# Kernel tuning notes

Measured on AMD Instinct MI355X. Metric: run time of the kernel, lower is better.

Reference implementation:

```python
import jax, jax.numpy as jnp
import numpy as np

# Dims (match init_kwargs / module defaults)
RD, PD = 128, 64          # residue_dim, pair_dim
H, QD, VD = 12, 32, 32    # num_heads, q_dim, v_dim
QP, VP = 8, 8             # num_q_points, num_v_points
LN_EPS = 1e-5
DIR_EPS = 1e-4
INF = 1e5


def _layer_norm(x, g, b):
    m = x.mean(-1, keepdims=True)
    v = ((x - m) ** 2).mean(-1, keepdims=True)
    return (x - m) * jax.lax.rsqrt(v + LN_EPS) * g + b


def setup_inputs() -> dict:
    key = jax.random.key(0)
    ks = jax.random.split(key, 24)
    N, L = 2, 512
    inp = {}
    inp['R'] = jax.random.normal(ks[0], (N, L, 3, 3), jnp.float32)
    inp['coord'] = jax.random.normal(ks[1], (N, L, 3), jnp.float32)
    inp['residue_feat'] = jax.random.normal(ks[2], (N, L, RD), jnp.float32)
    inp['pair_feat'] = jax.random.normal(ks[3], (N, L, L, PD), jnp.float32)
    inp['mask'] = jax.random.randint(ks[4], (N, L), 0, 2).astype(bool)

    def lin(k, fan_in, fan_out):  # torch nn.Linear default init, weight (out, in)
        lim = 1.0 / np.sqrt(fan_in)
        return jax.random.uniform(k, (fan_out, fan_in), jnp.float32, -lim, lim)

    inp['Wq'] = lin(ks[5], RD, QD * H)
    inp['Wk'] = lin(ks[6], RD, QD * H)
    inp['Wv'] = lin(ks[7], RD, VD * H)
    inp['Wpb'] = lin(ks[8], PD, H)
    inp['spatial_coef'] = jnp.full((1, 1, 1, H), np.log(np.exp(1.0) - 1.0), jnp.float32)
    inp['Wqp'] = lin(ks[9], RD, QP * H * 3)
    inp['Wkp'] = lin(ks[10], RD, QP * H * 3)
    inp['Wvp'] = lin(ks[11], RD, VP * H * 3)
    in_feat = H * VD + H * PD + H * VP * (3 + 3 + 1)  # 1824
    inp['Wout'] = lin(ks[12], in_feat, RD)
    inp['bout'] = jnp.zeros((RD,), jnp.float32)
    inp['Wm1'] = lin(ks[13], RD, RD)
    inp['bm1'] = jnp.zeros((RD,), jnp.float32)
    inp['Wm2'] = lin(ks[14], RD, RD)
    inp['bm2'] = jnp.zeros((RD,), jnp.float32)
    inp['Wm3'] = lin(ks[15], RD, RD)
    inp['bm3'] = jnp.zeros((RD,), jnp.float32)
    inp['ln1_g'] = jnp.ones((RD,), jnp.float32)
    inp['ln1_b'] = jnp.zeros((RD,), jnp.float32)
    inp['ln2_g'] = jnp.ones((RD,), jnp.float32)
    inp['ln2_b'] = jnp.zeros((RD,), jnp.float32)
    return inp


def _forward(R, coord, residue_feat, pair_feat, mask,
             Wq, Wk, Wv, Wpb, spatial_coef, Wqp, Wkp, Wvp,
             Wout, bout, Wm1, bm1, Wm2, bm2, Wm3, bm3,
             ln1_g, ln1_b, ln2_g, ln2_b):
    N, L, _ = residue_feat.shape

    def l2g(p):  # local->global: R @ p + t ; p: (N,L,M,3)
        return jnp.einsum('nlij,nlmj->nlmi', R, p) + coord[:, :, None, :]

    # --- node logits ---
    q = (residue_feat @ Wq.T).reshape(N, L, H, QD)
    k = (residue_feat @ Wk.T).reshape(N, L, H, QD)
    logits_node = jnp.einsum('nihd,njhd->nijh', q, k) * (1.0 / np.sqrt(QD))

    # --- pair logits ---
    logits_pair = pair_feat @ Wpb.T  # (N,L,L,H)

    # --- spatial logits ---
    qp = l2g((residue_feat @ Wqp.T).reshape(N, L, H * QP, 3)).reshape(N, L, H, QP * 3)
    kp = l2g((residue_feat @ Wkp.T).reshape(N, L, H * QP, 3)).reshape(N, L, H, QP * 3)
    # ||q_i - k_j||^2 = |q|^2 + |k|^2 - 2 q.k (avoids (N,L,L,H,3P) intermediate)
    qq = (qp ** 2).sum(-1)  # (N,L,H)
    kk = (kp ** 2).sum(-1)
    sum_sq = qq[:, :, None] + kk[:, None] - 2.0 * jnp.einsum('nihd,njhd->nijh', qp, kp)
    gamma = jax.nn.softplus(spatial_coef)  # (1,1,1,H)
    logits_spatial = sum_sq * (-gamma * np.sqrt(2.0 / (9.0 * QP)) / 2.0)

    logits = (logits_node + logits_pair + logits_spatial) * np.sqrt(1.0 / 3.0)

    # --- masked softmax over key axis (dim=2) ---
    mask_row = mask[:, :, None, None]            # (N,L,1,1)
    mask_pair = mask_row & mask[:, None, :, None]
    logits = jnp.where(mask_pair, logits, logits - INF)
    alpha = jax.nn.softmax(logits, axis=2)
    alpha = jnp.where(mask_row, alpha, 0.0)      # (N,L,L,H)

    # --- node aggregation ---
    v = (residue_feat @ Wv.T).reshape(N, L, H, VD)
    feat_node = jnp.einsum('nijh,njhd->nihd', alpha, v).reshape(N, L, H * VD)

    # --- pair aggregation ---
    feat_pair = jnp.einsum('nijh,nijc->nihc', alpha, pair_feat).reshape(N, L, H * PD)

    # --- spatial aggregation ---
    vp = l2g((residue_feat @ Wvp.T).reshape(N, L, H * VP, 3)).reshape(N, L, H, VP, 3)
    aggr = jnp.einsum('nijh,njhpc->nihpc', alpha, vp)  # (N,L,H,VP,3) global frame
    diff = aggr - coord[:, :, None, None, :]
    feat_points = jnp.einsum('nlji,nlhpj->nlhpi', R, diff)  # global->local: R^T (x - t)
    feat_dist = jnp.sqrt((feat_points ** 2).sum(-1))        # (N,L,H,VP)
    feat_dir = feat_points / (feat_dist[..., None] + DIR_EPS)
    feat_spatial = jnp.concatenate([
        feat_points.reshape(N, L, -1),
        feat_dist.reshape(N, L, -1),
        feat_dir.reshape(N, L, -1),
    ], axis=-1)

    feat_all = jnp.concatenate([feat_pair, feat_node, feat_spatial], axis=-1)
    feat_all = feat_all @ Wout.T + bout
    feat_all = jnp.where(mask[:, :, None], feat_all, 0.0)

    x = _layer_norm(residue_feat + feat_all, ln1_g, ln1_b)
    mlp = jax.nn.relu(jax.nn.relu(x @ Wm1.T + bm1) @ Wm2.T + bm2) @ Wm3.T + bm3
    return _layer_norm(x + mlp, ln2_g, ln2_b)


def reference(R, coord, residue_feat, pair_feat, mask,
              Wq, Wk, Wv, Wpb, spatial_coef, Wqp, Wkp, Wvp,
              Wout, bout, Wm1, bm1, Wm2, bm2, Wm3, bm3,
              ln1_g, ln1_b, ln2_g, ln2_b):
    return _forward(R, coord, residue_feat, pair_feat, mask,
                    Wq, Wk, Wv, Wpb, spatial_coef, Wqp, Wkp, Wvp,
                    Wout, bout, Wm1, bm1, Wm2, bm2, Wm3, bm3,
                    ln1_g, ln1_b, ln2_g, ln2_b)
```

## Files before the change

kernel.cpp:

```cpp
#include <hip/hip_runtime.h>
#include <hip/hip_bf16.h>

#define N_ 2
#define L_ 512
#define RD_ 128
#define PD_ 64
#define H_ 12
#define NL_ (N_*L_)
#define POUT_ 2016
#define FEAT_ 1824
#define INF_ 100000.0f
#define ISQD_ 0.17677669529663687f
#define ISQ3_ 0.5773502691896258f
#define LL_ ((size_t)L_*L_)

__global__ __launch_bounds__(256) void k_proj_gemm(
    const float* __restrict__ resf,
    const float* __restrict__ Wq, const float* __restrict__ Wk, const float* __restrict__ Wv,
    const float* __restrict__ Wqp, const float* __restrict__ Wkp, const float* __restrict__ Wvp,
    float* __restrict__ proj)
{
  const int rb = blockIdx.x * 8;
  const int ob = blockIdx.y * 128;
  const int tid = threadIdx.x;
  __shared__ float xt[8*132];
  __shared__ float wt[128*132];
  {
    int r = tid >> 5, kq = (tid & 31) * 4;
    float4 v = *(const float4*)(resf + (size_t)(rb + r)*RD_ + kq);
    xt[r*132+kq]=v.x; xt[r*132+kq+1]=v.y; xt[r*132+kq+2]=v.z; xt[r*132+kq+3]=v.w;
  }
  for (int m = 0; m < 16; ++m) {
    int idx = m*256 + tid;
    int r = idx >> 5, kq = (idx & 31) * 4;
    int o = ob + r;
    float4 v;
    if (o < 384)        v = *(const float4*)(Wq  + (size_t)o*RD_ + kq);
    else if (o < 768)   v = *(const float4*)(Wk  + (size_t)(o-384)*RD_ + kq);
    else if (o < 1152)  v = *(const float4*)(Wv  + (size_t)(o-768)*RD_ + kq);
    else if (o < 1440)  v = *(const float4*)(Wqp + (size_t)(o-1152)*RD_ + kq);
    else if (o < 1728)  v = *(const float4*)(Wkp + (size_t)(o-1440)*RD_ + kq);
    else if (o < POUT_) v = *(const float4*)(Wvp + (size_t)(o-1728)*RD_ + kq);
    else                v = make_float4(0.f,0.f,0.f,0.f);
    wt[r*132+kq]=v.x; wt[r*132+kq+1]=v.y; wt[r*132+kq+2]=v.z; wt[r*132+kq+3]=v.w;
  }
  __syncthreads();
  const int tt = tid & 7, g = tid >> 3;
  float acc0=0.f, acc1=0.f, acc2=0.f, acc3=0.f;
  #pragma unroll 4
  for (int k2 = 0; k2 < RD_; ++k2) {
    float xv = xt[tt*132 + k2];
    acc0 += xv * wt[(g     )*132 + k2];
    acc1 += xv * wt[(g + 32)*132 + k2];
    acc2 += xv * wt[(g + 64)*132 + k2];
    acc3 += xv * wt[(g + 96)*132 + k2];
  }
  float* dst = proj + (size_t)(rb + tt)*POUT_ + ob;
  if (ob + g      < POUT_) dst[g]      = acc0;
  if (ob + g + 32 < POUT_) dst[g+32]   = acc1;
  if (ob + g + 64 < POUT_) dst[g+64]   = acc2;
  if (ob + g + 96 < POUT_) dst[g+96]   = acc3;
}

__global__ __launch_bounds__(64) void k_rot(
    const float* __restrict__ R, const float* __restrict__ coord,
    const float* __restrict__ spc, const float* __restrict__ proj,
    float* __restrict__ qt, float* __restrict__ kt, float* __restrict__ vpg)
{
  const int t = blockIdx.x;
  const int n = t / L_, i = t % L_;
  const int tid = threadIdx.x;
  __shared__ float prow[POUT_];
  __shared__ float qpl[288], kpl[288], vpl[288];
  __shared__ float qqs[H_], kks[H_], coefs[H_];
  for (int m = tid; m < POUT_/4; m += 64)
    ((float4*)prow)[m] = *((const float4*)(proj + (size_t)t*POUT_) + m);
  if (tid < H_) coefs[tid] = -log1pf(expf(spc[tid])) * (1.0f/12.0f);
  __syncthreads();
  const float* Rm = R + (size_t)t*9;
  const float r00=Rm[0],r01=Rm[1],r02=Rm[2],r10=Rm[3],r11=Rm[4],r12=Rm[5],r20=Rm[6],r21=Rm[7],r22=Rm[8];
  const float cx = coord[(size_t)t*3], cy = coord[(size_t)t*3+1], cz = coord[(size_t)t*3+2];
  for (int idx = tid; idx < 288; idx += 64) {
    int mat = idx / 96, p = idx % 96;
    const float* s = prow + 1152 + mat*288 + p*3;
    float px=s[0], py=s[1], pz=s[2];
    float gx = r00*px + r01*py + r02*pz + cx;
    float gy = r10*px + r11*py + r12*pz + cy;
    float gz = r20*px + r21*py + r22*pz + cz;
    float* d = (mat==0? qpl : mat==1? kpl : vpl) + p*3;
    d[0]=gx; d[1]=gy; d[2]=gz;
  }
  __syncthreads();
  if (tid < 24) {
    int mat = tid / H_, h = tid % H_;
    const float* s = (mat==0? qpl : kpl) + h*24;
    float acc = 0.f;
    #pragma unroll
    for (int c2 = 0; c2 < 24; ++c2) acc += s[c2]*s[c2];
    (mat==0? qqs : kks)[h] = acc;
  }
  for (int m = tid; m < 72; m += 64)
    ((float4*)(vpg + (size_t)t*288))[m] = ((float4*)vpl)[m];
  __syncthreads();
  for (int idx = tid; idx < 2*H_*64; idx += 64) {
    int which = idx / 768, rem = idx % 768, h = rem >> 6, c = rem & 63;
    float val;
    if (which == 0) {
      if (c < 32)       val = prow[h*32 + c] * ISQD_;
      else if (c < 56)  val = qpl[h*24 + (c-32)] * (-2.0f * coefs[h]);
      else if (c == 56) val = coefs[h] * qqs[h];
      else if (c == 57) val = coefs[h];
      else              val = 0.f;
      qt[((size_t)(n*H_ + h)*L_ + i)*64 + c] = val;
    } else {
      if (c < 32)       val = prow[384 + h*32 + c];
      else if (c < 56)  val = kpl[h*24 + (c-32)];
      else if (c == 56) val = 1.0f;
      else if (c == 57) val = kks[h];
      else              val = 0.f;
      kt[((size_t)(n*H_ + h)*L_ + i)*64 + c] = val;
    }
  }
}

__global__ __launch_bounds__(256) void k_lgns(
    const float* __restrict__ qt, const float* __restrict__ kt,
    float* __restrict__ lgal)
{
  const int jb = blockIdx.x * 64, ib = blockIdx.y * 64, nh = blockIdx.z;
  const int tid = threadIdx.x;
  __shared__ float qs[64*66], ks[64*66];
  for (int m = 0; m < 4; ++m) {
    int idx = m*256 + tid;
    int r = idx >> 4, kq = (idx & 15) * 4;
    float4 a = *(const float4*)(qt + ((size_t)nh*L_ + ib + r)*64 + kq);
    qs[r*66+kq]=a.x; qs[r*66+kq+1]=a.y; qs[r*66+kq+2]=a.z; qs[r*66+kq+3]=a.w;
    float4 b = *(const float4*)(kt + ((size_t)nh*L_ + jb + r)*64 + kq);
    ks[r*66+kq]=b.x; ks[r*66+kq+1]=b.y; ks[r*66+kq+2]=b.z; ks[r*66+kq+3]=b.w;
  }
  __syncthreads();
  const int tx = tid & 15, ty = tid >> 4;
  const int i0 = ty*4, j0 = tx*4;
  float acc[4][4] = {};
  #pragma unroll 4
  for (int k2 = 0; k2 < 64; k2 += 2) {
    float2 qv[4], kv[4];
    #pragma unroll
    for (int d = 0; d < 4; ++d) {
      qv[d] = *(const float2*)(qs + (i0+d)*66 + k2);
      kv[d] = *(const float2*)(ks + (j0+d)*66 + k2);
    }
    #pragma unroll
    for (int a2 = 0; a2 < 4; ++a2)
      #pragma unroll
      for (int b2 = 0; b2 < 4; ++b2)
        acc[a2][b2] += qv[a2].x*kv[b2].x + qv[a2].y*kv[b2].y;
  }
  #pragma unroll
  for (int a2 = 0; a2 < 4; ++a2) {
    float4 v = make_float4(acc[a2][0], acc[a2][1], acc[a2][2], acc[a2][3]);
    *(float4*)(lgal + ((size_t)nh*L_ + ib + i0 + a2)*L_ + jb + j0) = v;
  }
}

__global__ __launch_bounds__(256) void k_pbias(
    const float* __restrict__ pair, const int* __restrict__ mask,
    const float* __restrict__ Wpb, float* __restrict__ lgal)
{
  const int jt2 = blockIdx.x, i = blockIdx.y, n = blockIdx.z;
  const int bi = n*L_ + i;
  const int tid = threadIdx.x;
  __shared__ float pt[2][64*67];
  const int sr = tid >> 4, scq = (tid & 15)*4;
  #pragma unroll
  for (int m = 0; m < 4; ++m) {
    int r = m*16 + sr;
    float4 v = *(const float4*)(pair + ((size_t)bi*L_ + jt2*128 + r)*PD_ + scq);
    float* d = pt[0] + r*67 + scq;
    d[0]=v.x; d[1]=v.y; d[2]=v.z; d[3]=v.w;
  }
  __syncthreads();
  float4 rg[4];
  #pragma unroll
  for (int m = 0; m < 4; ++m) {
    int r = m*16 + sr;
    rg[m] = *(const float4*)(pair + ((size_t)bi*L_ + jt2*128 + 64 + r)*PD_ + scq);
  }

  const int r = tid & 63;
  const int w = __builtin_amdgcn_readfirstlane(tid >> 6);
  const float* w0 = Wpb + (w    )*64;
  const float* w1 = Wpb + (w + 4)*64;
  const float* w2 = Wpb + (w + 8)*64;
  const int mi = mask[bi];

  {
    const int j = jt2*128 + r;
    const float* pr = pt[0] + r*67;
    float a0=0.f, a1=0.f, a2=0.f;
    #pragma unroll 16
    for (int c = 0; c < 64; ++c) {
      float pv = pr[c];
      a0 += pv*w0[c]; a1 += pv*w1[c]; a2 += pv*w2[c];
    }
    const float mt = (mi && mask[n*L_ + j]) ? 0.f : -INF_;
    size_t base = ((size_t)(n*H_ + w)*L_ + i)*L_ + j;
    float l0 = lgal[base], l1 = lgal[base + 4*LL_], l2 = lgal[base + 8*LL_];
    lgal[base        ] = (l0 + a0)*ISQ3_ + mt;
    lgal[base + 4*LL_] = (l1 + a1)*ISQ3_ + mt;
    lgal[base + 8*LL_] = (l2 + a2)*ISQ3_ + mt;
  }

  #pragma unroll
  for (int m = 0; m < 4; ++m) {
    int rr = m*16 + sr;
    float* d = pt[1] + rr*67 + scq;
    d[0]=rg[m].x; d[1]=rg[m].y; d[2]=rg[m].z; d[3]=rg[m].w;
  }
  __syncthreads();
  {
    const int j = jt2*128 + 64 + r;
    const float* pr = pt[1] + r*67;
    float a0=0.f, a1=0.f, a2=0.f;
    #pragma unroll 16
    for (int c = 0; c < 64; ++c) {
      float pv = pr[c];
      a0 += pv*w0[c]; a1 += pv*w1[c]; a2 += pv*w2[c];
    }
    const float mt = (mi && mask[n*L_ + j]) ? 0.f : -INF_;
    size_t base = ((size_t)(n*H_ + w)*L_ + i)*L_ + j;
    float l0 = lgal[base], l1 = lgal[base + 4*LL_], l2 = lgal[base + 8*LL_];
    lgal[base        ] = (l0 + a0)*ISQ3_ + mt;
    lgal[base + 4*LL_] = (l1 + a1)*ISQ3_ + mt;
    lgal[base + 8*LL_] = (l2 + a2)*ISQ3_ + mt;
  }
}

__global__ __launch_bounds__(256) void k_softx(
    const int* __restrict__ mask, float* __restrict__ lgal)
{
  const int tid = threadIdx.x;
  const int wid = tid >> 6, lane = tid & 63;
  const int rid = blockIdx.x*4 + wid;
  const int i = rid & (L_-1);
  const int nh = rid >> 9;
  const int n = nh / H_;
  float4* r4 = (float4*)(lgal + (size_t)rid * L_);
  float4 p0 = r4[lane], p1 = r4[lane + 64];
  float mx = fmaxf(fmaxf(fmaxf(p0.x,p0.y),fmaxf(p0.z,p0.w)),
                   fmaxf(fmaxf(p1.x,p1.y),fmaxf(p1.z,p1.w)));
  #pragma unroll
  for (int off = 1; off < 64; off <<= 1) mx = fmaxf(mx, __shfl_xor(mx, off, 64));
  p0.x = expf(p0.x - mx); p0.y = expf(p0.y - mx);
  p0.z = expf(p0.z - mx); p0.w = expf(p0.w - mx);
  p1.x = expf(p1.x - mx); p1.y = expf(p1.y - mx);
  p1.z = expf(p1.z - mx); p1.w = expf(p1.w - mx);
  float s = p0.x+p0.y+p0.z+p0.w + p1.x+p1.y+p1.z+p1.w;
  #pragma unroll
  for (int off = 1; off < 64; off <<= 1) s += __shfl_xor(s, off, 64);
  const float inv = (mask[n*L_ + i] ? 1.f : 0.f) / s;
  p0.x*=inv; p0.y*=inv; p0.z*=inv; p0.w*=inv;
  p1.x*=inv; p1.y*=inv; p1.z*=inv; p1.w*=inv;
  r4[lane] = p0; r4[lane + 64] = p1;
}

__global__ __launch_bounds__(256) void k_paggr(
    const float* __restrict__ pair, const float* __restrict__ lgal,
    float* __restrict__ feat)
{
  const int i = blockIdx.x, n = blockIdx.y;
  const int bi = n*L_ + i;
  const int tid = threadIdx.x;
  const int w = tid >> 6, l = tid & 63;
  const int js = l >> 4, cq = (l & 15) << 2;
  __shared__ float part[4][H_][64];

  const float* pb = pair + ((size_t)bi*L_ + w*128 + js)*PD_ + cq;
  const float* ab[H_];
  #pragma unroll
  for (int h = 0; h < H_; ++h)
    ab[h] = lgal + ((size_t)(n*H_ + h)*L_ + i)*L_ + w*128 + js;

  float4 acc[H_];
  #pragma unroll
  for (int h = 0; h < H_; ++h) acc[h] = make_float4(0.f,0.f,0.f,0.f);

  #pragma unroll 2
  for (int g = 0; g < 32; ++g) {
    float4 pv = *(const float4*)(pb + (size_t)g*4*PD_);
    #pragma unroll
    for (int h = 0; h < H_; ++h) {
      float av = ab[h][g*4];
      acc[h].x += av*pv.x; acc[h].y += av*pv.y;
      acc[h].z += av*pv.z; acc[h].w += av*pv.w;
    }
  }

  #pragma unroll
  for (int h = 0; h < H_; ++h) {
    acc[h].x += __shfl_xor(acc[h].x, 16, 64);
    acc[h].y += __shfl_xor(acc[h].y, 16, 64);
    acc[h].z += __shfl_xor(acc[h].z, 16, 64);
    acc[h].w += __shfl_xor(acc[h].w, 16, 64);
    acc[h].x += __shfl_xor(acc[h].x, 32, 64);
    acc[h].y += __shfl_xor(acc[h].y, 32, 64);
    acc[h].z += __shfl_xor(acc[h].z, 32, 64);
    acc[h].w += __shfl_xor(acc[h].w, 32, 64);
  }
  if (l < 16) {
    #pragma unroll
    for (int h = 0; h < H_; ++h)
      *(float4*)(&part[w][h][cq]) = acc[h];
  }
  __syncthreads();
  for (int u = tid; u < H_*64; u += 256) {
    int h = u >> 6, c = u & 63;
    feat[(size_t)bi*FEAT_ + h*64 + c] =
        part[0][h][c] + part[1][h][c] + part[2][h][c] + part[3][h][c];
  }
}

__global__ __launch_bounds__(256) void k_av(
    const float* __restrict__ lgal, const float* __restrict__ proj,
    const float* __restrict__ vpg, float* __restrict__ pav)
{
  const int ib = blockIdx.x * 64;
  const int nh = blockIdx.y;
  const int z  = blockIdx.z;
  const int jb = z*64;
  const int n = nh / H_, h = nh % H_, nL = n*L_;
  const int tid = threadIdx.x;
  __shared__ float as[64*66];
  __shared__ float bs[64*60];
  const int tx = tid & 15, ty = tid >> 4;
  const int i0 = ty*4, c0 = tx*4;
  for (int m = 0; m < 4; ++m) {
    int idx = m*256 + tid;
    int r = idx >> 4, jq = (idx & 15) * 4;
    float4 a = *(const float4*)(lgal + ((size_t)nh*L_ + ib + r)*L_ + jb + jq);
    as[r*66+jq]=a.x; as[r*66+jq+1]=a.y; as[r*66+jq+2]=a.z; as[r*66+jq+3]=a.w;
  }
  for (int m = 0; m < 4; ++m) {
    int idx = m*256 + tid;
    int j = idx >> 4, qq = idx & 15;
    if (qq < 14) {
      float4 v;
      if (qq < 8) v = *(const float4*)(proj + (size_t)(nL + jb + j)*POUT_ + 768 + h*32 + qq*4);
      else        v = *(const float4*)(vpg  + (size_t)(nL + jb + j)*288  + h*24 + (qq-8)*4);
      float* d = bs + j*60 + qq*4;
      d[0]=v.x; d[1]=v.y; d[2]=v.z; d[3]=v.w;
    }
  }
  __syncthreads();
  float acc[4][4] = {};
  #pragma unroll 4
  for (int k2 = 0; k2 < 64; k2 += 2) {
    float2 av[4];
    #pragma unroll
    for (int d = 0; d < 4; ++d) av[d] = *(const float2*)(as + (i0+d)*66 + k2);
    float4 bv0 = *(const float4*)(bs + (k2  )*60 + c0);
    float4 bv1 = *(const float4*)(bs + (k2+1)*60 + c0);
    #pragma unroll
    for (int a2 = 0; a2 < 4; ++a2) {
      acc[a2][0] += av[a2].x*bv0.x + av[a2].y*bv1.x;
      acc[a2][1] += av[a2].x*bv0.y + av[a2].y*bv1.y;
      acc[a2][2] += av[a2].x*bv0.z + av[a2].y*bv1.z;
      acc[a2][3] += av[a2].x*bv0.w + av[a2].y*bv1.w;
    }
  }
  if (c0 < 56) {
    #pragma unroll
    for (int a2 = 0; a2 < 4; ++a2)
      *(float4*)(pav + (((size_t)z*24 + nh)*L_ + ib + i0 + a2)*56 + c0) =
          make_float4(acc[a2][0], acc[a2][1], acc[a2][2], acc[a2][3]);
  }
}

__global__ __launch_bounds__(256) void k_avred(
    const float* __restrict__ pav, const float* __restrict__ R,
    const float* __restrict__ coord, float* __restrict__ feat)
{
  const int tok = blockIdx.x, tid = threadIdx.x;
  const int n = tok / L_, i = tok % L_;
  __shared__ float ag[288];
  float* fb = feat + (size_t)tok*FEAT_;
  const size_t zstride = (size_t)24*L_*56;
  for (int u = tid; u < 672; u += 256) {
    int h = u / 56, c = u % 56;
    size_t base = (((size_t)(n*H_ + h))*L_ + i)*56 + c;
    float v = 0.f;
    #pragma unroll
    for (int zz = 0; zz < 8; ++zz) v += pav[base + zz*zstride];
    if (c < 32) fb[768 + h*32 + c] = v;
    else        ag[h*24 + (c - 32)] = v;
  }
  __syncthreads();
  if (tid < 96) {
    const float* Rm = R + (size_t)tok*9;
    const float cx = coord[(size_t)tok*3], cy = coord[(size_t)tok*3+1], cz = coord[(size_t)tok*3+2];
    float dx = ag[tid*3] - cx, dy = ag[tid*3+1] - cy, dz = ag[tid*3+2] - cz;
    float fx = Rm[0]*dx + Rm[3]*dy + Rm[6]*dz;
    float fy = Rm[1]*dx + Rm[4]*dy + Rm[7]*dz;
    float fz = Rm[2]*dx + Rm[5]*dy + Rm[8]*dz;
    float dist = sqrtf(fx*fx + fy*fy + fz*fz);
    float idn = 1.f/(dist + 1e-4f);
    fb[1152+tid*3]=fx; fb[1152+tid*3+1]=fy; fb[1152+tid*3+2]=fz;
    fb[1440+tid]=dist;
    fb[1536+tid*3]=fx*idn; fb[1536+tid*3+1]=fy*idn; fb[1536+tid*3+2]=fz*idn;
  }
}

__global__ __launch_bounds__(256) void k_y_gemm(
    const float* __restrict__ feat, const float* __restrict__ Wout,
    float* __restrict__ ybuf)
{
  const int rb = blockIdx.x * 8;
  const int ob = blockIdx.y * 64;
  const int tid = threadIdx.x;
  __shared__ float wt[96*65];
  __shared__ float ft[96*10];
  const int o = tid & 63, tg = tid >> 6;
  float acc0 = 0.f, acc1 = 0.f;
  for (int kb = 0; kb < FEAT_; kb += 96) {
    for (int m = 0; m < 6; ++m) {
      int idx = m*256 + tid;
      int r = idx / 24, cq = (idx % 24) * 4;
      float4 v = *(const float4*)(Wout + (size_t)(ob + r)*FEAT_ + kb + cq);
      wt[(cq  )*65 + r] = v.x;
      wt[(cq+1)*65 + r] = v.y;
      wt[(cq+2)*65 + r] = v.z;
      wt[(cq+3)*65 + r] = v.w;
    }
    if (tid < 192) {
      int t = tid / 24, cq = (tid % 24) * 4;
      float4 v = *(const float4*)(feat + (size_t)(rb + t)*FEAT_ + kb + cq);
      ft[(cq  )*10 + t] = v.x;
      ft[(cq+1)*10 + t] = v.y;
      ft[(cq+2)*10 + t] = v.z;
      ft[(cq+3)*10 + t] = v.w;
    }
    __syncthreads();
    #pragma unroll 4
    for (int k2 = 0; k2 < 96; ++k2) {
      float wv = wt[k2*65 + o];
      float2 fv = *(const float2*)(ft + k2*10 + tg*2);
      acc0 += wv * fv.x;
      acc1 += wv * fv.y;
    }
    __syncthreads();
  }
  ybuf[(size_t)(rb + tg*2    )*RD_ + ob + o] = acc0;
  ybuf[(size_t)(rb + tg*2 + 1)*RD_ + ob + o] = acc1;
}

__device__ __forceinline__ float bsum128(float v, float* red, int tid) {
  #pragma unroll
  for (int off = 1; off < 64; off <<= 1) v += __shfl_xor(v, off, 64);
  __syncthreads();
  if ((tid & 63) == 0) red[tid >> 6] = v;
  __syncthreads();
  return red[0] + red[1];
}

__global__ __launch_bounds__(128) void k_mlp(
    const float* __restrict__ resf, const int* __restrict__ mask,
    const float* __restrict__ ybuf, const float* __restrict__ bout,
    const float* __restrict__ Wm1, const float* __restrict__ bm1,
    const float* __restrict__ Wm2, const float* __restrict__ bm2,
    const float* __restrict__ Wm3, const float* __restrict__ bm3,
    const float* __restrict__ g1, const float* __restrict__ b1,
    const float* __restrict__ g2, const float* __restrict__ b2,
    float* __restrict__ out)
{
  const int t = blockIdx.x, tid = threadIdx.x;
  __shared__ float xb[RD_], h1b[RD_], h2b[RD_];
  __shared__ float red[2];
  float acc = ybuf[(size_t)t*RD_ + tid] + bout[tid];
  if (mask[t] == 0) acc = 0.f;
  float r = resf[(size_t)t*RD_ + tid] + acc;

  float mean = bsum128(r, red, tid) * (1.f/RD_);
  float d = r - mean;
  float var = bsum128(d*d, red, tid) * (1.f/RD_);
  float xn = d * rsqrtf(var + 1e-5f) * g1[tid] + b1[tid];
  xb[tid] = xn;
  __syncthreads();

  float a1 = bm1[tid];
  {
    const float4* w4 = (const float4*)(Wm1 + (size_t)tid*RD_);
    #pragma unroll
    for (int c = 0; c < RD_/4; ++c) { float4 a = w4[c]; a1 += a.x*xb[4*c]+a.y*xb[4*c+1]+a.z*xb[4*c+2]+a.w*xb[4*c+3]; }
  }
  a1 = fmaxf(a1, 0.f);
  h1b[tid] = a1;
  __syncthreads();

  float a2 = bm2[tid];
  {
    const float4* w4 = (const float4*)(Wm2 + (size_t)tid*RD_);
    #pragma unroll
    for (int c = 0; c < RD_/4; ++c) { float4 a = w4[c]; a2 += a.x*h1b[4*c]+a.y*h1b[4*c+1]+a.z*h1b[4*c+2]+a.w*h1b[4*c+3]; }
  }
  a2 = fmaxf(a2, 0.f);
  h2b[tid] = a2;
  __syncthreads();

  float a3 = bm3[tid];
  {
    const float4* w4 = (const float4*)(Wm3 + (size_t)tid*RD_);
    #pragma unroll
    for (int c = 0; c < RD_/4; ++c) { float4 a = w4[c]; a3 += a.x*h2b[4*c]+a.y*h2b[4*c+1]+a.z*h2b[4*c+2]+a.w*h2b[4*c+3]; }
  }
  float r2 = xn + a3;
  float mean2 = bsum128(r2, red, tid) * (1.f/RD_);
  float d2 = r2 - mean2;
  float var2 = bsum128(d2*d2, red, tid) * (1.f/RD_);
  out[(size_t)t*RD_ + tid] = d2 * rsqrtf(var2 + 1e-5f) * g2[tid] + b2[tid];
}

extern "C" void kernel_launch(void* const* d_in, const int* in_sizes, int n_in,
                              void* d_out, int out_size, void* d_ws, size_t ws_size,
                              hipStream_t stream) {
  (void)in_sizes; (void)n_in; (void)out_size; (void)ws_size;
  const float* R     = (const float*)d_in[0];
  const float* coord = (const float*)d_in[1];
  const float* resf  = (const float*)d_in[2];
  const float* pair  = (const float*)d_in[3];
  const int*   mask  = (const int*)  d_in[4];
  const float* Wq    = (const float*)d_in[5];
  const float* Wk    = (const float*)d_in[6];
  const float* Wv    = (const float*)d_in[7];
  const float* Wpb   = (const float*)d_in[8];
  const float* spc   = (const float*)d_in[9];
  const float* Wqp   = (const float*)d_in[10];
  const float* Wkp   = (const float*)d_in[11];
  const float* Wvp   = (const float*)d_in[12];
  const float* Wout  = (const float*)d_in[13];
  const float* bout  = (const float*)d_in[14];
  const float* Wm1   = (const float*)d_in[15];
  const float* bm1   = (const float*)d_in[16];
  const float* Wm2   = (const float*)d_in[17];
  const float* bm2   = (const float*)d_in[18];
  const float* Wm3   = (const float*)d_in[19];
  const float* bm3   = (const float*)d_in[20];
  const float* g1    = (const float*)d_in[21];
  const float* b1    = (const float*)d_in[22];
  const float* g2    = (const float*)d_in[23];
  const float* b2    = (const float*)d_in[24];

  float* ws   = (float*)d_ws;
  float* proj = ws;
  float* qt   = proj + (size_t)NL_*POUT_;
  float* kt   = qt   + (size_t)N_*H_*L_*64;
  float* vpg  = kt   + (size_t)N_*H_*L_*64;
  float* lgal = vpg  + (size_t)NL_*288;
  float* feat = lgal + (size_t)N_*H_*L_*L_;
  float* ybuf = feat + (size_t)NL_*FEAT_;
  float* pav  = ybuf + (size_t)NL_*RD_;

  k_proj_gemm<<<dim3(NL_/8, 16), 256, 0, stream>>>(resf, Wq, Wk, Wv, Wqp, Wkp, Wvp, proj);
  k_rot<<<NL_, 64, 0, stream>>>(R, coord, spc, proj, qt, kt, vpg);
  k_lgns<<<dim3(L_/64, L_/64, N_*H_), 256, 0, stream>>>(qt, kt, lgal);
  k_pbias<<<dim3(L_/128, L_, N_), 256, 0, stream>>>(pair, mask, Wpb, lgal);
  k_softx<<<(N_*H_*L_)/4, 256, 0, stream>>>(mask, lgal);
  k_paggr<<<dim3(L_, N_), 256, 0, stream>>>(pair, lgal, feat);
  k_av<<<dim3(L_/64, N_*H_, 8), 256, 0, stream>>>(lgal, proj, vpg, pav);
  k_avred<<<NL_, 256, 0, stream>>>(pav, R, coord, feat);
  k_y_gemm<<<dim3(NL_/8, 2), 256, 0, stream>>>(feat, Wout, ybuf);
  k_mlp<<<NL_, 128, 0, stream>>>(resf, mask, ybuf, bout, Wm1, bm1, Wm2, bm2, Wm3, bm3,
                                 g1, b1, g2, b2, (float*)d_out);
}
```

Baseline: 243.9 us.

## Vectorize loads in proj GEMM, pair-bias and pair-aggregation kernels

```diff
diff --git a/kernel.cpp b/kernel.cpp
--- a/kernel.cpp
+++ b/kernel.cpp
@@ -48,12 +48,16 @@
   const int tt = tid & 7, g = tid >> 3;
   float acc0=0.f, acc1=0.f, acc2=0.f, acc3=0.f;
   #pragma unroll 4
-  for (int k2 = 0; k2 < RD_; ++k2) {
-    float xv = xt[tt*132 + k2];
-    acc0 += xv * wt[(g     )*132 + k2];
-    acc1 += xv * wt[(g + 32)*132 + k2];
-    acc2 += xv * wt[(g + 64)*132 + k2];
-    acc3 += xv * wt[(g + 96)*132 + k2];
+  for (int k2 = 0; k2 < RD_; k2 += 2) {
+    float2 xv = *(const float2*)(xt + tt*132 + k2);
+    float2 w0 = *(const float2*)(wt + (g     )*132 + k2);
+    float2 w1 = *(const float2*)(wt + (g + 32)*132 + k2);
+    float2 w2 = *(const float2*)(wt + (g + 64)*132 + k2);
+    float2 w3 = *(const float2*)(wt + (g + 96)*132 + k2);
+    acc0 += xv.x*w0.x + xv.y*w0.y;
+    acc1 += xv.x*w1.x + xv.y*w1.y;
+    acc2 += xv.x*w2.x + xv.y*w2.y;
+    acc3 += xv.x*w3.x + xv.y*w3.y;
   }
   float* dst = proj + (size_t)(rb + tt)*POUT_ + ob;
   if (ob + g      < POUT_) dst[g]      = acc0;
@@ -167,72 +171,53 @@
     const float* __restrict__ pair, const int* __restrict__ mask,
     const float* __restrict__ Wpb, float* __restrict__ lgal)
 {
-  const int jt2 = blockIdx.x, i = blockIdx.y, n = blockIdx.z;
+  const int jt = blockIdx.x, i = blockIdx.y, n = blockIdx.z;
   const int bi = n*L_ + i;
   const int tid = threadIdx.x;
-  __shared__ float pt[2][64*67];
-  const int sr = tid >> 4, scq = (tid & 15)*4;
-  #pragma unroll
-  for (int m = 0; m < 4; ++m) {
-    int r = m*16 + sr;
-    float4 v = *(const float4*)(pair + ((size_t)bi*L_ + jt2*128 + r)*PD_ + scq);
-    float* d = pt[0] + r*67 + scq;
-    d[0]=v.x; d[1]=v.y; d[2]=v.z; d[3]=v.w;
-  }
-  __syncthreads();
-  float4 rg[4];
-  #pragma unroll
-  for (int m = 0; m < 4; ++m) {
-    int r = m*16 + sr;
-    rg[m] = *(const float4*)(pair + ((size_t)bi*L_ + jt2*128 + 64 + r)*PD_ + scq);
-  }
-
-  const int r = tid & 63;
-  const int w = __builtin_amdgcn_readfirstlane(tid >> 6);
-  const float* w0 = Wpb + (w    )*64;
-  const float* w1 = Wpb + (w + 4)*64;
-  const float* w2 = Wpb + (w + 8)*64;
+  const int w = tid >> 6, l = tid & 63;
+  const int js = l >> 4, cq = (l & 15) << 2;
+  const float4 wp0 = *(const float4*)(Wpb + (w    )*64 + cq);
+  const float4 wp1 = *(const float4*)(Wpb + (w + 4)*64 + cq);
+  const float4 wp2 = *(const float4*)(Wpb + (w + 8)*64 + cq);
   const int mi = mask[bi];
-
-  {
-    const int j = jt2*128 + r;
-    const float* pr = pt[0] + r*67;
-    float a0=0.f, a1=0.f, a2=0.f;
-    #pragma unroll 16
-    for (int c = 0; c < 64; ++c) {
-      float pv = pr[c];
-      a0 += pv*w0[c]; a1 += pv*w1[c]; a2 += pv*w2[c];
-    }
-    const float mt = (mi && mask[n*L_ + j]) ? 0.f : -INF_;
-    size_t base = ((size_t)(n*H_ + w)*L_ + i)*L_ + j;
-    float l0 = lgal[base], l1 = lgal[base + 4*LL_], l2 = lgal[base + 8*LL_];
-    lgal[base        ] = (l0 + a0)*ISQ3_ + mt;
-    lgal[base + 4*LL_] = (l1 + a1)*ISQ3_ + mt;
-    lgal[base + 8*LL_] = (l2 + a2)*ISQ3_ + mt;
-  }
-
-  #pragma unroll
-  for (int m = 0; m < 4; ++m) {
-    int rr = m*16 + sr;
-    float* d = pt[1] + rr*67 + scq;
-    d[0]=rg[m].x; d[1]=rg[m].y; d[2]=rg[m].z; d[3]=rg[m].w;
-  }
-  __syncthreads();
-  {
-    const int j = jt2*128 + 64 + r;
-    const float* pr = pt[1] + r*67;
-    float a0=0.f, a1=0.f, a2=0.f;
-    #pragma unroll 16
-    for (int c = 0; c < 64; ++c) {
-      float pv = pr[c];
-      a0 += pv*w0[c]; a1 += pv*w1[c]; a2 += pv*w2[c];
-    }
-    const float mt = (mi && mask[n*L_ + j]) ? 0.f : -INF_;
-    size_t base = ((size_t)(n*H_ + w)*L_ + i)*L_ + j;
-    float l0 = lgal[base], l1 = lgal[base + 4*LL_], l2 = lgal[base + 8*LL_];
-    lgal[base        ] = (l0 + a0)*ISQ3_ + mt;
-    lgal[base + 4*LL_] = (l1 + a1)*ISQ3_ + mt;
-    lgal[base + 8*LL_] = (l2 + a2)*ISQ3_ + mt;
+  const float* prow = pair + (size_t)bi*L_*PD_;
+  for (int g = 0; g < 8; ++g) {
+    const int j0 = jt*128 + g*16 + js*4;
+    float s0[4], s1[4], s2[4];
+    #pragma unroll
+    for (int t = 0; t < 4; ++t) {
+      float4 pv = *(const float4*)(prow + (size_t)(j0+t)*PD_ + cq);
+      s0[t] = pv.x*wp0.x + pv.y*wp0.y + pv.z*wp0.z + pv.w*wp0.w;
+      s1[t] = pv.x*wp1.x + pv.y*wp1.y + pv.z*wp1.z + pv.w*wp1.w;
+      s2[t] = pv.x*wp2.x + pv.y*wp2.y + pv.z*wp2.z + pv.w*wp2.w;
+    }
+    #pragma unroll
+    for (int off = 1; off < 16; off <<= 1) {
+      #pragma unroll
+      for (int t = 0; t < 4; ++t) {
+        s0[t] += __shfl_xor(s0[t], off, 64);
+        s1[t] += __shfl_xor(s1[t], off, 64);
+        s2[t] += __shfl_xor(s2[t], off, 64);
+      }
+    }
+    const int hq = l & 15;
+    if (hq < 3) {
+      const int h = w + hq*4;
+      size_t base = (((size_t)(n*H_ + h))*L_ + i)*L_ + j0;
+      float4 lv = *(float4*)(lgal + base);
+      float4 sv = (hq == 0) ? make_float4(s0[0],s0[1],s0[2],s0[3])
+                : (hq == 1) ? make_float4(s1[0],s1[1],s1[2],s1[3])
+                :             make_float4(s2[0],s2[1],s2[2],s2[3]);
+      float m0 = (mi && mask[n*L_ + j0    ]) ? 0.f : -INF_;
+      float m1 = (mi && mask[n*L_ + j0 + 1]) ? 0.f : -INF_;
+      float m2 = (mi && mask[n*L_ + j0 + 2]) ? 0.f : -INF_;
+      float m3 = (mi && mask[n*L_ + j0 + 3]) ? 0.f : -INF_;
+      lv.x = (lv.x + sv.x)*ISQ3_ + m0;
+      lv.y = (lv.y + sv.y)*ISQ3_ + m1;
+      lv.z = (lv.z + sv.z)*ISQ3_ + m2;
+      lv.w = (lv.w + sv.w)*ISQ3_ + m3;
+      *(float4*)(lgal + base) = lv;
+    }
   }
 }
 
@@ -275,24 +260,26 @@
   const int js = l >> 4, cq = (l & 15) << 2;
   __shared__ float part[4][H_][64];
 
-  const float* pb = pair + ((size_t)bi*L_ + w*128 + js)*PD_ + cq;
-  const float* ab[H_];
-  #pragma unroll
-  for (int h = 0; h < H_; ++h)
-    ab[h] = lgal + ((size_t)(n*H_ + h)*L_ + i)*L_ + w*128 + js;
+  const float* prow = pair + (size_t)bi*L_*PD_;
+  const float* arow = lgal + ((size_t)(n*H_)*L_ + i)*L_;
 
   float4 acc[H_];
   #pragma unroll
   for (int h = 0; h < H_; ++h) acc[h] = make_float4(0.f,0.f,0.f,0.f);
 
-  #pragma unroll 2
-  for (int g = 0; g < 32; ++g) {
-    float4 pv = *(const float4*)(pb + (size_t)g*4*PD_);
+  for (int g = 0; g < 8; ++g) {
+    const int j0 = w*128 + g*16 + js*4;
+    float4 pv0 = *(const float4*)(prow + (size_t)(j0  )*PD_ + cq);
+    float4 pv1 = *(const float4*)(prow + (size_t)(j0+1)*PD_ + cq);
+    float4 pv2 = *(const float4*)(prow + (size_t)(j0+2)*PD_ + cq);
+    float4 pv3 = *(const float4*)(prow + (size_t)(j0+3)*PD_ + cq);
     #pragma unroll
     for (int h = 0; h < H_; ++h) {
-      float av = ab[h][g*4];
-      acc[h].x += av*pv.x; acc[h].y += av*pv.y;
-      acc[h].z += av*pv.z; acc[h].w += av*pv.w;
+      float4 a4 = *(const float4*)(arow + (size_t)h*LL_ + j0);
+      acc[h].x += a4.x*pv0.x + a4.y*pv1.x + a4.z*pv2.x + a4.w*pv3.x;
+      acc[h].y += a4.x*pv0.y + a4.y*pv1.y + a4.z*pv2.y + a4.w*pv3.y;
+      acc[h].z += a4.x*pv0.z + a4.y*pv1.z + a4.z*pv2.z + a4.w*pv3.z;
+      acc[h].w += a4.x*pv0.w + a4.y*pv1.w + a4.z*pv2.w + a4.w*pv3.w;
     }
   }
 
```

Result: slower. 298.9 us (+22.6%).
